# Kernel optimization log

Measured on AMD Instinct MI355X. Metric: run time of the kernel, lower is better.

The kernel has to match this reference:

```python
import jax, jax.numpy as jnp
import numpy as np

# Config derived from init_kwargs
VOCAB_FACTORS = (16, 16, 16, 16)   # 16^4 = 65536 = resonant vocab for 50000
D_FACTORS = (8, 8, 4, 4)           # prod = 1024 = d_model
RANK = 16
D_MODEL = 1024


def setup_inputs() -> dict:
    key = jax.random.key(0)
    ks = jax.random.split(key, 6)
    input_ids = jax.random.randint(ks[0], (8, 2048), 0, 50000, dtype=jnp.int64)
    scale = 0.02 / np.sqrt(4.0)  # orthogonal-init scale / sqrt(num_cores)
    core0 = jax.random.normal(ks[1], (16, 1, RANK, 8), dtype=jnp.float32) * scale
    core1 = jax.random.normal(ks[2], (16, RANK, RANK, 8), dtype=jnp.float32) * scale
    core2 = jax.random.normal(ks[3], (16, RANK, RANK, 4), dtype=jnp.float32) * scale
    core3 = jax.random.normal(ks[4], (16, RANK, 1, 4), dtype=jnp.float32) * scale
    # phase init: 2*pi*(i+1)/log(i+2) mod 2*pi
    i = jnp.arange(RANK, dtype=jnp.float32)
    phase_shift = jnp.mod(2.0 * jnp.pi * (i + 1.0) / jnp.log(i + 2.0), 2.0 * jnp.pi)
    return {"input_ids": input_ids, "core0": core0, "core1": core1,
            "core2": core2, "core3": core3, "phase_shift": phase_shift}


def _decompose(flat_ids):
    # big-endian mixed-radix decomposition over VOCAB_FACTORS
    strides = []
    s = 1
    for v in reversed(VOCAB_FACTORS):
        strides.append(s)
        s *= v
    strides = strides[::-1]
    return [(flat_ids // st) % v for st, v in zip(strides, VOCAB_FACTORS)]


def _forward(input_ids, cores, phase_shift):
    B, S = input_ids.shape
    flat = input_ids.reshape(-1)                     # (N,)
    idxs = _decompose(flat)
    # first core: (N, 1, r, d0) -> (N, r, d0)
    res = cores[0][idxs[0]][:, 0]
    # phase rotation on the rank bond channels
    res = res * jnp.cos(phase_shift)[None, :, None]
    N = flat.shape[0]
    for k in range(1, len(cores)):
        g = cores[k][idxs[k]]                        # (N, r_l, r_r, d_k)
        res = jnp.einsum('nrD,nrsd->nsDd', res, g)   # chain small-rank contraction
        res = res.reshape(N, g.shape[2], -1)
    return res.reshape(B, S, D_MODEL)


def reference(input_ids, core0, core1, core2, core3, phase_shift):
    return _forward(input_ids, (core0, core1, core2, core3), phase_shift)
```

## Files before the change

kernel.cpp:

```cpp
#include <hip/hip_runtime.h>


typedef float f32x4 __attribute__((ext_vector_type(4)));

__global__ __launch_bounds__(256) void k_tables(
    const float* __restrict__ core0, const float* __restrict__ core1,
    const float* __restrict__ core2, const float* __restrict__ core3,
    const float* __restrict__ phase,
    float* __restrict__ T, float* __restrict__ F)
{
  const int gid = blockIdx.x * 256 + threadIdx.x;
  const int lane = threadIdx.x & 63;
  const float cown = cosf(phase[lane & 15]);
  if (blockIdx.x < 1024) {
    const int p01 = gid >> 10, r = gid & 1023;
    const int b = r >> 6, u = r & 63;
    const int D0 = u >> 3, d1 = u & 7;
    const int i0 = p01 >> 4, i1 = p01 & 15;
    const float* c0 = core0 + i0 * 128 + D0;
    const float* c1 = core1 + i1 * 2048 + b * 8 + d1;
    float acc = 0.f;
    #pragma unroll
    for (int a = 0; a < 16; ++a) {
      const float ca = __shfl(cown, a, 16);
      acc += c0[a * 8] * ca * c1[a * 128];
    }
    const int us = (u >> 4) + (u & 15) * 4;
    T[p01 * 1024 + b * 64 + us] = acc;
  } else {
    const int o = gid - 262144;
    const int p23 = o >> 8, r = o & 255;
    const int b = r >> 4, v = r & 15;
    const int d2 = v >> 2, d3 = v & 3;
    const int i2 = p23 >> 4, i3 = p23 & 15;
    const float* c2 = core2 + i2 * 1024 + b * 64 + d2;
    const float* c3 = core3 + i3 * 64 + d3;
    float acc = 0.f;
    #pragma unroll
    for (int c = 0; c < 16; ++c)
      acc += c2[c * 4] * c3[c * 4];
    F[p23 * 256 + b * 16 + v] = acc;
  }
}

__global__ __launch_bounds__(256) void k_out9(
    const int* __restrict__ ids, const float* __restrict__ T,
    const float* __restrict__ F, float* __restrict__ out)
{
  __shared__ float sF[4][256];
  const int wv = threadIdx.x >> 6, lane = threadIdx.x & 63;
  const int n = blockIdx.x * 4 + wv;
  const int id = ids[n];
  const int p01 = id >> 8, p23 = id & 255;
  const int ug = lane >> 2, vg = lane & 3;

  f32x4 treg[16];
  const float* Tp = T + p01 * 1024 + ug * 4;
  #pragma unroll
  for (int b = 0; b < 16; ++b)
    treg[b] = *reinterpret_cast<const f32x4*>(Tp + b * 64);

  float* tF = sF[wv];
  {
    const f32x4 v = *reinterpret_cast<const f32x4*>(F + p23 * 256 + lane * 4);
    *reinterpret_cast<f32x4*>(tF + lane * 4) = v;
  }
  __syncthreads();

  float acc[4][4];
  #pragma unroll
  for (int i = 0; i < 4; ++i)
    #pragma unroll
    for (int j = 0; j < 4; ++j) acc[i][j] = 0.f;

  #pragma unroll
  for (int b = 0; b < 16; ++b) {
    const f32x4 f = *reinterpret_cast<const f32x4*>(tF + b * 16 + vg * 4);
    const f32x4 t = treg[b];
    acc[0][0] += t.x*f.x; acc[0][1] += t.x*f.y; acc[0][2] += t.x*f.z; acc[0][3] += t.x*f.w;
    acc[1][0] += t.y*f.x; acc[1][1] += t.y*f.y; acc[1][2] += t.y*f.z; acc[1][3] += t.y*f.w;
    acc[2][0] += t.z*f.x; acc[2][1] += t.z*f.y; acc[2][2] += t.z*f.z; acc[2][3] += t.z*f.w;
    acc[3][0] += t.w*f.x; acc[3][1] += t.w*f.y; acc[3][2] += t.w*f.z; acc[3][3] += t.w*f.w;
  }

  float* op = out + (size_t)n * 1024 + lane * 4;
  #pragma unroll
  for (int e = 0; e < 4; ++e) {
    f32x4 v4 = { acc[e][0], acc[e][1], acc[e][2], acc[e][3] };
    *reinterpret_cast<f32x4*>(op + e * 256) = v4;
  }
}

extern "C" void kernel_launch(void* const* d_in, const int* in_sizes, int n_in,
                              void* d_out, int out_size, void* d_ws, size_t ws_size,
                              hipStream_t stream) {
  const int*   ids   = (const int*)  d_in[0];
  const float* core0 = (const float*)d_in[1];
  const float* core1 = (const float*)d_in[2];
  const float* core2 = (const float*)d_in[3];
  const float* core3 = (const float*)d_in[4];
  const float* phase = (const float*)d_in[5];
  float* out = (float*)d_out;

  float* Tt = (float*)d_ws;
  float* Ft = (float*)d_ws + 262144;

  const int tokens = in_sizes[0];
  hipLaunchKernelGGL(k_tables, dim3(1280), dim3(256), 0, stream,
                     core0, core1, core2, core3, phase, Tt, Ft);
  hipLaunchKernelGGL(k_out9, dim3(tokens / 4), dim3(256), 0, stream,
                     ids, Tt, Ft, out);
}
```

Measured before the change: 25.26 us.

## Process two tokens per wavefront with 4x8 register tiles and nontemporal stores

The output kernel now assigns two tokens to each 64-lane wavefront. Each lane computes a 4x8 tile instead of 4x4, which halves the block count and doubles the per-thread FMA work relative to loads. Output writes switch to nontemporal stores so the 64 MB streaming output does not pollute cache. The larger accumulator array raises register pressure, and each lane now writes 32-byte contiguous chunks, which changes store coalescing.

```diff
diff --git a/kernel.cpp b/kernel.cpp
--- a/kernel.cpp
+++ b/kernel.cpp
@@ -43,51 +43,62 @@
   }
 }
 
-__global__ __launch_bounds__(256) void k_out9(
+__global__ __launch_bounds__(256) void k_outA(
     const int* __restrict__ ids, const float* __restrict__ T,
     const float* __restrict__ F, float* __restrict__ out)
 {
-  __shared__ float sF[4][256];
+  __shared__ float sF[4][512];
   const int wv = threadIdx.x >> 6, lane = threadIdx.x & 63;
-  const int n = blockIdx.x * 4 + wv;
-  const int id = ids[n];
+  const int tok = lane >> 5;
+  const int l31 = lane & 31;
+  const int r   = lane & 15;
+  const int vh  = (lane >> 4) & 1;
+  const int n   = blockIdx.x * 8 + wv * 2 + tok;
+  const int id  = ids[n];
   const int p01 = id >> 8, p23 = id & 255;
-  const int ug = lane >> 2, vg = lane & 3;
 
   f32x4 treg[16];
-  const float* Tp = T + p01 * 1024 + ug * 4;
+  const float* Tp = T + p01 * 1024 + r * 4;
   #pragma unroll
   for (int b = 0; b < 16; ++b)
     treg[b] = *reinterpret_cast<const f32x4*>(Tp + b * 64);
 
-  float* tF = sF[wv];
-  {
-    const f32x4 v = *reinterpret_cast<const f32x4*>(F + p23 * 256 + lane * 4);
-    *reinterpret_cast<f32x4*>(tF + lane * 4) = v;
+  float* tF = &sF[wv][tok * 256];
+  #pragma unroll
+  for (int c = 0; c < 2; ++c) {
+    const f32x4 v = *reinterpret_cast<const f32x4*>(F + p23 * 256 + c * 128 + l31 * 4);
+    *reinterpret_cast<f32x4*>(tF + c * 128 + l31 * 4) = v;
   }
   __syncthreads();
 
-  float acc[4][4];
+  float acc[4][8];
   #pragma unroll
-  for (int i = 0; i < 4; ++i)
+  for (int k = 0; k < 4; ++k)
     #pragma unroll
-    for (int j = 0; j < 4; ++j) acc[i][j] = 0.f;
+    for (int j = 0; j < 8; ++j) acc[k][j] = 0.f;
 
   #pragma unroll
   for (int b = 0; b < 16; ++b) {
-    const f32x4 f = *reinterpret_cast<const f32x4*>(tF + b * 16 + vg * 4);
+    const f32x4 f0 = *reinterpret_cast<const f32x4*>(tF + b * 16 + vh * 8);
+    const f32x4 f1 = *reinterpret_cast<const f32x4*>(tF + b * 16 + vh * 8 + 4);
     const f32x4 t = treg[b];
-    acc[0][0] += t.x*f.x; acc[0][1] += t.x*f.y; acc[0][2] += t.x*f.z; acc[0][3] += t.x*f.w;
-    acc[1][0] += t.y*f.x; acc[1][1] += t.y*f.y; acc[1][2] += t.y*f.z; acc[1][3] += t.y*f.w;
-    acc[2][0] += t.z*f.x; acc[2][1] += t.z*f.y; acc[2][2] += t.z*f.z; acc[2][3] += t.z*f.w;
-    acc[3][0] += t.w*f.x; acc[3][1] += t.w*f.y; acc[3][2] += t.w*f.z; acc[3][3] += t.w*f.w;
+    #pragma unroll
+    for (int k = 0; k < 4; ++k) {
+      const float tk = (k == 0) ? t.x : (k == 1) ? t.y : (k == 2) ? t.z : t.w;
+      acc[k][0] += tk * f0.x; acc[k][1] += tk * f0.y;
+      acc[k][2] += tk * f0.z; acc[k][3] += tk * f0.w;
+      acc[k][4] += tk * f1.x; acc[k][5] += tk * f1.y;
+      acc[k][6] += tk * f1.z; acc[k][7] += tk * f1.w;
+    }
   }
 
-  float* op = out + (size_t)n * 1024 + lane * 4;
+  float* op = out + (size_t)n * 1024 + r * 16 + vh * 8;
   #pragma unroll
-  for (int e = 0; e < 4; ++e) {
-    f32x4 v4 = { acc[e][0], acc[e][1], acc[e][2], acc[e][3] };
-    *reinterpret_cast<f32x4*>(op + e * 256) = v4;
+  for (int k = 0; k < 4; ++k) {
+    f32x4 lo = { acc[k][0], acc[k][1], acc[k][2], acc[k][3] };
+    f32x4 hi = { acc[k][4], acc[k][5], acc[k][6], acc[k][7] };
+    __builtin_nontemporal_store(lo, reinterpret_cast<f32x4*>(op + k * 256));
+    __builtin_nontemporal_store(hi, reinterpret_cast<f32x4*>(op + k * 256 + 4));
   }
 }
 
@@ -108,6 +119,6 @@
   const int tokens = in_sizes[0];
   hipLaunchKernelGGL(k_tables, dim3(1280), dim3(256), 0, stream,
                      core0, core1, core2, core3, phase, Tt, Ft);
-  hipLaunchKernelGGL(k_out9, dim3(tokens / 4), dim3(256), 0, stream,
+  hipLaunchKernelGGL(k_outA, dim3(tokens / 8), dim3(256), 0, stream,
                      ids, Tt, Ft, out);
 }
```

Result: slower. 30.73 us (+21.7%).

## Remap output kernel: per-lane T column, scalar F loads, LDS transpose, nontemporal stores

Applied to the files above, without the earlier changes.

Each lane of the output kernel now holds one column of the T table, 16 floats with coalesced scalar loads. Since p23 is made wave-uniform through readfirstlane, the F row is read directly from global memory as broadcast loads instead of being staged through LDS first. Each lane computes 16 outputs, writes them to a padded LDS tile for transposition, then emits coalesced 16-byte nontemporal stores. The T table layout drops its prior swizzle to match. This trades the F staging for an output transpose through LDS, and the nontemporal stores are meant to keep the 64 MB output stream from polluting the cache.

```diff
diff --git a/kernel.cpp b/kernel.cpp
--- a/kernel.cpp
+++ b/kernel.cpp
@@ -25,8 +25,7 @@
       const float ca = __shfl(cown, a, 16);
       acc += c0[a * 8] * ca * c1[a * 128];
     }
-    const int us = (u >> 4) + (u & 15) * 4;
-    T[p01 * 1024 + b * 64 + us] = acc;
+    T[p01 * 1024 + b * 64 + u] = acc;
   } else {
     const int o = gid - 262144;
     const int p23 = o >> 8, r = o & 255;
@@ -43,51 +42,59 @@
   }
 }
 
-__global__ __launch_bounds__(256) void k_out9(
+__global__ __launch_bounds__(256) void k_outB(
     const int* __restrict__ ids, const float* __restrict__ T,
     const float* __restrict__ F, float* __restrict__ out)
 {
-  __shared__ float sF[4][256];
+  __shared__ float xp[4][64 * 20];
   const int wv = threadIdx.x >> 6, lane = threadIdx.x & 63;
   const int n = blockIdx.x * 4 + wv;
   const int id = ids[n];
-  const int p01 = id >> 8, p23 = id & 255;
-  const int ug = lane >> 2, vg = lane & 3;
+  const int p01 = id >> 8;
+  const int p23 = __builtin_amdgcn_readfirstlane(id & 255);
+  const float* __restrict__ Fp = F + p23 * 256;
 
-  f32x4 treg[16];
-  const float* Tp = T + p01 * 1024 + ug * 4;
+  float treg[16];
+  const float* Tp = T + p01 * 1024 + lane;
   #pragma unroll
   for (int b = 0; b < 16; ++b)
-    treg[b] = *reinterpret_cast<const f32x4*>(Tp + b * 64);
+    treg[b] = Tp[b * 64];
 
-  float* tF = sF[wv];
-  {
-    const f32x4 v = *reinterpret_cast<const f32x4*>(F + p23 * 256 + lane * 4);
-    *reinterpret_cast<f32x4*>(tF + lane * 4) = v;
+  float acc[16];
+  #pragma unroll
+  for (int v = 0; v < 16; ++v) acc[v] = 0.f;
+
+  #pragma unroll
+  for (int b = 0; b < 16; ++b) {
+    const f32x4 f0 = *reinterpret_cast<const f32x4*>(Fp + b * 16);
+    const f32x4 f1 = *reinterpret_cast<const f32x4*>(Fp + b * 16 + 4);
+    const f32x4 f2 = *reinterpret_cast<const f32x4*>(Fp + b * 16 + 8);
+    const f32x4 f3 = *reinterpret_cast<const f32x4*>(Fp + b * 16 + 12);
+    const float tb = treg[b];
+    acc[0]  = fmaf(tb, f0.x, acc[0]);  acc[1]  = fmaf(tb, f0.y, acc[1]);
+    acc[2]  = fmaf(tb, f0.z, acc[2]);  acc[3]  = fmaf(tb, f0.w, acc[3]);
+    acc[4]  = fmaf(tb, f1.x, acc[4]);  acc[5]  = fmaf(tb, f1.y, acc[5]);
+    acc[6]  = fmaf(tb, f1.z, acc[6]);  acc[7]  = fmaf(tb, f1.w, acc[7]);
+    acc[8]  = fmaf(tb, f2.x, acc[8]);  acc[9]  = fmaf(tb, f2.y, acc[9]);
+    acc[10] = fmaf(tb, f2.z, acc[10]); acc[11] = fmaf(tb, f2.w, acc[11]);
+    acc[12] = fmaf(tb, f3.x, acc[12]); acc[13] = fmaf(tb, f3.y, acc[13]);
+    acc[14] = fmaf(tb, f3.z, acc[14]); acc[15] = fmaf(tb, f3.w, acc[15]);
+  }
+
+  float* xw = xp[wv];
+  #pragma unroll
+  for (int e = 0; e < 4; ++e) {
+    f32x4 w = { acc[e*4+0], acc[e*4+1], acc[e*4+2], acc[e*4+3] };
+    *reinterpret_cast<f32x4*>(xw + lane * 20 + e * 4) = w;
   }
   __syncthreads();
 
-  float acc[4][4];
-  #pragma unroll
-  for (int i = 0; i < 4; ++i)
-    #pragma unroll
-    for (int j = 0; j < 4; ++j) acc[i][j] = 0.f;
-
-  #pragma unroll
-  for (int b = 0; b < 16; ++b) {
-    const f32x4 f = *reinterpret_cast<const f32x4*>(tF + b * 16 + vg * 4);
-    const f32x4 t = treg[b];
-    acc[0][0] += t.x*f.x; acc[0][1] += t.x*f.y; acc[0][2] += t.x*f.z; acc[0][3] += t.x*f.w;
-    acc[1][0] += t.y*f.x; acc[1][1] += t.y*f.y; acc[1][2] += t.y*f.z; acc[1][3] += t.y*f.w;
-    acc[2][0] += t.z*f.x; acc[2][1] += t.z*f.y; acc[2][2] += t.z*f.z; acc[2][3] += t.z*f.w;
-    acc[3][0] += t.w*f.x; acc[3][1] += t.w*f.y; acc[3][2] += t.w*f.z; acc[3][3] += t.w*f.w;
-  }
-
   float* op = out + (size_t)n * 1024 + lane * 4;
   #pragma unroll
-  for (int e = 0; e < 4; ++e) {
-    f32x4 v4 = { acc[e][0], acc[e][1], acc[e][2], acc[e][3] };
-    *reinterpret_cast<f32x4*>(op + e * 256) = v4;
+  for (int k = 0; k < 4; ++k) {
+    const f32x4 r = *reinterpret_cast<const f32x4*>(
+        xw + (k * 16 + (lane >> 2)) * 20 + (lane & 3) * 4);
+    __builtin_nontemporal_store(r, reinterpret_cast<f32x4*>(op + k * 256));
   }
 }
 
@@ -108,6 +115,6 @@
   const int tokens = in_sizes[0];
   hipLaunchKernelGGL(k_tables, dim3(1280), dim3(256), 0, stream,
                      core0, core1, core2, core3, phase, Tt, Ft);
-  hipLaunchKernelGGL(k_out9, dim3(tokens / 4), dim3(256), 0, stream,
+  hipLaunchKernelGGL(k_outB, dim3(tokens / 4), dim3(256), 0, stream,
                      ids, Tt, Ft, out);
 }
```

Result: faster. 24.70 us (-2.2%).
